# Performance work log

Measured on AMD Instinct MI355X. Metric: run time of the kernel, lower is better.

Reference implementation:

```python
import jax, jax.numpy as jnp
import numpy as np

B, T, DIM = 256, 2048, 64
THETA, MU, SIGMA = 0.1, 0.0, 1.0


def setup_inputs() -> dict:
    key = jax.random.key(0)
    k1, k2 = jax.random.split(key)
    # strictly increasing positive times, shape [B, T, 1]
    dt = jax.random.uniform(k1, (B, T, 1), minval=1e-3, maxval=1e-2, dtype=jnp.float32)
    ts = jnp.cumsum(dt, axis=1)
    # standard normal reparameterization noise for Normal(0, delta_ts).rsample()
    noise = jax.random.normal(k2, (B, T, DIM), dtype=jnp.float32)
    return {"ts": ts, "noise": noise}


def reference(ts, noise):
    h = DIM // 2  # slice_index
    # t_prev: 0 at step 0, ts[:, :-1] afterwards
    t_prev = jnp.concatenate([jnp.zeros_like(ts[:, :1]), ts[:, :-1]], axis=1)  # [B,T,1]
    # Brownian-increment std: sqrt(t_k - t_{k-1})  (sqrt(t_0) at k=0)
    db = jnp.sqrt(ts - t_prev)  # [B,T,1]
    # OU-increment std: sqrt(exp(2*theta*t_k) - exp(2*theta*t_{k-1}))  (exp(0)=1 at k=0)
    dou = jnp.sqrt(jnp.exp(2.0 * THETA * ts) - jnp.exp(2.0 * THETA * t_prev))  # [B,T,1]
    bt = ts.shape[:-1]
    delta = jnp.concatenate([jnp.broadcast_to(db, bt + (h,)),
                             jnp.broadcast_to(dou, bt + (h,))], axis=-1)  # [B,T,DIM]
    invalid = delta <= 0.0
    delta = jnp.where(invalid, delta + 1e-4, delta)
    # rsample = 0 + delta * eps; zero out invalid entries
    r = jnp.where(invalid, 0.0, delta * noise)
    # per-half scaling
    scale = jnp.concatenate([jnp.full((h,), np.sqrt(SIGMA), dtype=r.dtype),
                             jnp.full((h,), SIGMA / np.sqrt(2.0 * THETA), dtype=r.dtype)])
    r = r * scale
    out = jnp.cumsum(r, axis=-2)  # scan along time
    # OU mean-reversion transform on second half
    e = jnp.exp(-THETA * ts)  # [B,T,1]
    ou = e * out[..., h:] + MU * (1.0 - e)
    # normalize=True branch
    bm = out[..., :h] / (SIGMA * jnp.sqrt(ts) + 1e-8)
    ou = ou / (SIGMA * jnp.sqrt((1.0 - jnp.exp(-2.0 * THETA * ts)) / (2.0 * THETA)) + 1e-8)
    return jnp.concatenate([bm, ou], axis=-1)  # [B,T,DIM]
```

## Files before the change

### kernel.cpp

```cpp
#include <hip/hip_runtime.h>
#include <cstddef>

#define B_   256
#define T_   2048
#define DIM_ 64
#define HD_  (DIM_ / 2)
#define SGN_ 128
#define SPT_ (T_ / SGN_)
#define OU_SCALE 2.2360679774997896f

__global__ __launch_bounds__(1024, 8) void fused_kernel(
        const float* __restrict__ ts,
        const float* __restrict__ noise,
        float* __restrict__ out)
{
    __shared__ float2 cofs[T_];
    __shared__ float4 par[SGN_][8];

    const int bid = blockIdx.x;
    const int b   = bid >> 1;
    const int h   = bid & 1;
    const int tid = threadIdx.x;
    const int sg  = tid >> 3;
    const int qi  = tid & 7;
    const int q   = (h << 5) + (qi << 2);

    const float* tsb = ts + (size_t)b * T_;
    for (int t = tid; t < T_; t += 1024) {
        const float tk = tsb[t];
        const float tp = (t == 0) ? 0.0f : tsb[t - 1];
        float d, f;
        if (h == 0) {
            const float db = sqrtf(tk - tp);
            d = (db <= 0.0f) ? 0.0f : db;
            f = 1.0f / (sqrtf(tk) + 1e-8f);
        } else {
            const float dou = sqrtf(expf(0.2f * tp) * expm1f(0.2f * (tk - tp)));
            d = (dou <= 0.0f) ? 0.0f : dou * OU_SCALE;
            const float em = expf(-0.1f * tk);
            f = em / (sqrtf(-expm1f(-0.2f * tk) * 5.0f) + 1e-8f);
        }
        cofs[t] = make_float2(d, f);
    }
    __syncthreads();

    const size_t rowbase = (size_t)b * T_ * DIM_;
    const int    tb      = sg * SPT_;
    const float* np = noise + rowbase + (size_t)tb * DIM_ + q;

    {
        float4 a = make_float4(0.f, 0.f, 0.f, 0.f);
#pragma unroll
        for (int i = 0; i < SPT_; ++i) {
            const float4 v = *(const float4*)(np + (size_t)i * DIM_);
            const float  d = cofs[tb + i].x;
            a.x = fmaf(d, v.x, a.x);
            a.y = fmaf(d, v.y, a.y);
            a.z = fmaf(d, v.z, a.z);
            a.w = fmaf(d, v.w, a.w);
        }
        par[sg][qi] = a;
    }
    __syncthreads();

    float4 acc = make_float4(0.f, 0.f, 0.f, 0.f);
    for (int k = 0; k < sg; ++k) {
        const float4 p = par[k][qi];
        acc.x += p.x; acc.y += p.y; acc.z += p.z; acc.w += p.w;
    }

    float* op = out + rowbase + (size_t)tb * DIM_ + q;
#pragma unroll
    for (int i = 0; i < SPT_; ++i) {
        const float4 v = *(const float4*)(np + (size_t)i * DIM_);
        const float2 c = cofs[tb + i];
        acc.x = fmaf(c.x, v.x, acc.x);
        acc.y = fmaf(c.x, v.y, acc.y);
        acc.z = fmaf(c.x, v.z, acc.z);
        acc.w = fmaf(c.x, v.w, acc.w);
        *(float4*)(op + (size_t)i * DIM_) =
            make_float4(acc.x * c.y, acc.y * c.y, acc.z * c.y, acc.w * c.y);
    }
}

extern "C" void kernel_launch(void* const* d_in, const int* in_sizes, int n_in,
                              void* d_out, int out_size, void* d_ws, size_t ws_size,
                              hipStream_t stream) {
    const float* ts    = (const float*)d_in[0];
    const float* noise = (const float*)d_in[1];
    float* out = (float*)d_out;
    (void)d_ws; (void)ws_size; (void)in_sizes; (void)n_in; (void)out_size;

    fused_kernel<<<B_ * 2, 1024, 0, stream>>>(ts, noise, out);
}
```

Measured before the change: 251.9 us.

## Replace two-pass segmented scan with streaming tiled scan using wave shuffles

Each block now walks the time axis in 16 tiles of 128 steps, using wave shuffles and a small shared-memory table of per-wave totals to scan each tile, then carries a running base into the next tile. Noise is read once and prefetched two tiles ahead, instead of being read twice with strided per-thread segments. The aim is to halve global reads and give coalesced access across consecutive time rows. In exchange it adds two block-wide barriers per tile and a 16-entry reduction per thread per tile.

Measured after the change: 251.2 us. About the same (-0.3%).

```diff
diff --git a/kernel.cpp b/kernel.cpp
--- a/kernel.cpp
+++ b/kernel.cpp
@@ -4,26 +4,28 @@
 #define B_   256
 #define T_   2048
 #define DIM_ 64
-#define HD_  (DIM_ / 2)
-#define SGN_ 128
-#define SPT_ (T_ / SGN_)
+#define NT_  16
+#define TS_  128
 #define OU_SCALE 2.2360679774997896f
 
-__global__ __launch_bounds__(1024, 8) void fused_kernel(
+__global__ __launch_bounds__(1024, 8) void stream_kernel(
         const float* __restrict__ ts,
         const float* __restrict__ noise,
         float* __restrict__ out)
 {
     __shared__ float2 cofs[T_];
-    __shared__ float4 par[SGN_][8];
+    __shared__ float4 wtot[16][9];
 
-    const int bid = blockIdx.x;
-    const int b   = bid >> 1;
-    const int h   = bid & 1;
-    const int tid = threadIdx.x;
-    const int sg  = tid >> 3;
-    const int qi  = tid & 7;
-    const int q   = (h << 5) + (qi << 2);
+    const int bid  = blockIdx.x;
+    const int b    = bid >> 1;
+    const int h    = bid & 1;
+    const int tid  = threadIdx.x;
+    const int st   = tid >> 3;
+    const int qi   = tid & 7;
+    const int q    = (h << 5) + (qi << 2);
+    const int w    = tid >> 6;
+    const int sl   = st & 7;
+    const int lane = tid & 63;
 
     const float* tsb = ts + (size_t)b * T_;
     for (int t = tid; t < T_; t += 1024) {
@@ -45,41 +47,56 @@
     __syncthreads();
 
     const size_t rowbase = (size_t)b * T_ * DIM_;
-    const int    tb      = sg * SPT_;
-    const float* np = noise + rowbase + (size_t)tb * DIM_ + q;
+    const float* np = noise + rowbase + q;
+    float*       op = out   + rowbase + q;
 
-    {
-        float4 a = make_float4(0.f, 0.f, 0.f, 0.f);
+    float4 v0 = *(const float4*)(np + (size_t)(0 * TS_ + st) * DIM_);
+    float4 v1 = *(const float4*)(np + (size_t)(1 * TS_ + st) * DIM_);
+
+    float4 base = make_float4(0.f, 0.f, 0.f, 0.f);
+
+    for (int j = 0; j < NT_; ++j) {
+        float4 v2 = make_float4(0.f, 0.f, 0.f, 0.f);
+        if (j + 2 < NT_)
+            v2 = *(const float4*)(np + (size_t)((j + 2) * TS_ + st) * DIM_);
+
+        const int    t = j * TS_ + st;
+        const float2 c = cofs[t];
+
+        float4 s = make_float4(c.x * v0.x, c.x * v0.y, c.x * v0.z, c.x * v0.w);
+
 #pragma unroll
-        for (int i = 0; i < SPT_; ++i) {
-            const float4 v = *(const float4*)(np + (size_t)i * DIM_);
-            const float  d = cofs[tb + i].x;
-            a.x = fmaf(d, v.x, a.x);
-            a.y = fmaf(d, v.y, a.y);
-            a.z = fmaf(d, v.z, a.z);
-            a.w = fmaf(d, v.w, a.w);
+        for (int d = 1; d <= 4; d <<= 1) {
+            const int src = lane - (d << 3);
+            const float tx = __shfl(s.x, src, 64);
+            const float ty = __shfl(s.y, src, 64);
+            const float tz = __shfl(s.z, src, 64);
+            const float tw = __shfl(s.w, src, 64);
+            if (sl >= d) { s.x += tx; s.y += ty; s.z += tz; s.w += tw; }
         }
-        par[sg][qi] = a;
-    }
-    __syncthreads();
 
-    float4 acc = make_float4(0.f, 0.f, 0.f, 0.f);
-    for (int k = 0; k < sg; ++k) {
-        const float4 p = par[k][qi];
-        acc.x += p.x; acc.y += p.y; acc.z += p.z; acc.w += p.w;
-    }
+        if (sl == 7) wtot[w][qi] = s;
+        __syncthreads();
 
-    float* op = out + rowbase + (size_t)tb * DIM_ + q;
+        float4 wb = make_float4(0.f, 0.f, 0.f, 0.f);
+        float4 tt = make_float4(0.f, 0.f, 0.f, 0.f);
 #pragma unroll
-    for (int i = 0; i < SPT_; ++i) {
-        const float4 v = *(const float4*)(np + (size_t)i * DIM_);
-        const float2 c = cofs[tb + i];
-        acc.x = fmaf(c.x, v.x, acc.x);
-        acc.y = fmaf(c.x, v.y, acc.y);
-        acc.z = fmaf(c.x, v.z, acc.z);
-        acc.w = fmaf(c.x, v.w, acc.w);
-        *(float4*)(op + (size_t)i * DIM_) =
-            make_float4(acc.x * c.y, acc.y * c.y, acc.z * c.y, acc.w * c.y);
+        for (int k = 0; k < 16; ++k) {
+            const float4 p = wtot[k][qi];
+            if (k < w) { wb.x += p.x; wb.y += p.y; wb.z += p.z; wb.w += p.w; }
+            tt.x += p.x; tt.y += p.y; tt.z += p.z; tt.w += p.w;
+        }
+
+        const float f = c.y;
+        const float4 o = make_float4((base.x + wb.x + s.x) * f,
+                                     (base.y + wb.y + s.y) * f,
+                                     (base.z + wb.z + s.z) * f,
+                                     (base.w + wb.w + s.w) * f);
+        *(float4*)(op + (size_t)t * DIM_) = o;
+
+        base.x += tt.x; base.y += tt.y; base.z += tt.z; base.w += tt.w;
+        __syncthreads();
+        v0 = v1; v1 = v2;
     }
 }
 
@@ -91,5 +108,5 @@
     float* out = (float*)d_out;
     (void)d_ws; (void)ws_size; (void)in_sizes; (void)n_in; (void)out_size;
 
-    fused_kernel<<<B_ * 2, 1024, 0, stream>>>(ts, noise, out);
+    stream_kernel<<<B_ * 2, 1024, 0, stream>>>(ts, noise, out);
 }
```
